# Kernel optimization log

Measured on AMD Instinct MI355X. Metric: run time of the kernel, lower is better.

Reference implementation:

```python
import jax, jax.numpy as jnp
import numpy as np

K = 4  # spline order (degree K-1)


def bspline_basis(x, t, k):
    """Evaluate the k nonzero B-spline basis functions of order k at x.

    x: [B, I] floats; t: [G+2k-1] clamped knot vector.
    Returns (idx [B,I,k] int32 basis indices, basis [B,I,k] values),
    using the de Boor / NURBS-book triangular recursion (vectorized over B,I;
    Python loops only over the small fixed order k).
    """
    m = t.shape[0]
    # interval index: t[i] <= x < t[i+1], clamped to valid span [k-1, m-k-1]
    i = jnp.clip(jnp.searchsorted(t, x, side='right') - 1, k - 1, m - k - 1)
    p = k - 1
    N = [jnp.ones_like(x)]
    left, right = [], []
    for j in range(1, p + 1):
        left.append(x - t[i + 1 - j])
        right.append(t[i + j] - x)
        saved = jnp.zeros_like(x)
        Nn = []
        for r in range(j):
            temp = N[r] / (right[r] + left[j - 1 - r])
            Nn.append(saved + right[r] * temp)
            saved = left[j - 1 - r] * temp
        Nn.append(saved)
        N = Nn
    idx = jnp.stack([i - p + j for j in range(k)], axis=-1)   # [B,I,k]
    basis = jnp.stack(N, axis=-1)                             # [B,I,k]
    return idx, basis


def setup_inputs() -> dict:
    key = jax.random.key(0)
    k1, k2 = jax.random.split(key)
    B, I, O, G, k = 2048, 128, 128, 64, K
    t0, t1 = -1.0, 1.0
    x = jax.random.uniform(k1, (B, I), jnp.float32, minval=t0, maxval=t1)
    # xavier_normal_ for fan_in=in_dim, fan_out=out_dim (per-slice heuristic)
    std = (2.0 / (I + O)) ** 0.5
    w = jax.random.normal(k2, (G + k, I, O), jnp.float32) * std
    t = jnp.concatenate([
        jnp.full((k - 1,), t0, jnp.float32),
        jnp.linspace(t0, t1, G + 1, dtype=jnp.float32),
        jnp.full((k - 1,), t1, jnp.float32),
    ])
    return {"x": x, "w": w, "t": t}


def reference(x, w, t):
    k = K
    B, I = x.shape
    O = w.shape[2]
    idx, basis = bspline_basis(x, t, k)                       # [B,I,k]
    # activation slot uses the last row of w (torch index -1)
    act_idx = jnp.full((B, I, 1), w.shape[0] - 1, idx.dtype)
    idx_full = jnp.concatenate([idx, act_idx], axis=-1)       # [B,I,k+1]
    y = jnp.concatenate([basis, jax.nn.silu(x)[..., None]], axis=-1)  # [B,I,k+1]
    wt = jnp.transpose(w, (1, 0, 2))                          # [I, G+k, O]
    w2 = wt[jnp.arange(I)[None, :, None], idx_full]           # [B,I,k+1,O] gather
    return jnp.einsum('bij,bijo->bo', y, w2)                  # [B,O]
```

## Files before the change

kernel.cpp:

```cpp
#include <hip/hip_runtime.h>
#include <math.h>

#define B_TOTAL 2048
#define I_DIM   128
#define O_DIM   128
#define GK      68
#define NKNOT   71
#define W_ELEMS ((size_t)GK * I_DIM * O_DIM)
#define WS_MIN  (W_ELEMS * 2)

__device__ __forceinline__ float rdlanef(float v, int l) {
    return __int_as_float(__builtin_amdgcn_readlane(__float_as_int(v), l));
}
__device__ __forceinline__ unsigned short f2bf(float f) {
    unsigned u = __float_as_uint(f);
    return (unsigned short)((u + 0x7fffu + ((u >> 16) & 1u)) >> 16);
}
__device__ __forceinline__ float bflo(unsigned u) { return __uint_as_float(u << 16); }
__device__ __forceinline__ float bfhi(unsigned u) { return __uint_as_float(u & 0xffff0000u); }

__global__ __launch_bounds__(256)
void wcvt(const float* __restrict__ w, unsigned short* __restrict__ wbf) {
    const int tid = threadIdx.x;
    const int p   = blockIdx.x * 8 + (tid >> 5);
    const int oq  = (tid & 31) * 4;
    const int g   = p >> 7;
    const int i   = p & 127;
    const float4 v = *(const float4*)(w + (size_t)p * O_DIM + oq);
    ushort4 o4;
    o4.x = f2bf(v.x); o4.y = f2bf(v.y); o4.z = f2bf(v.z); o4.w = f2bf(v.w);
    *(ushort4*)(wbf + ((size_t)i * GK + g) * O_DIM + oq) = o4;
}

__global__ __launch_bounds__(256, 8)
void flashkan_gather(const float* __restrict__ x,
                     const unsigned short* __restrict__ wbf,
                     const float* __restrict__ t,
                     float* __restrict__ out) {
    __shared__ float t_sh[NKNOT];
    __shared__ float psum[4][O_DIM];

    const int tid  = threadIdx.x;
    const int b    = blockIdx.x;
    const int wave = tid >> 6;
    const int lane = tid & 63;
    const int l32  = lane & 31;

    if (tid < NKNOT) t_sh[tid] = t[tid];
    __syncthreads();

    float cf0, cf1, cf2, cf3, cf4;
    int   cg;
    {
        const float xv = x[(size_t)b * I_DIM + wave * 32 + l32];

        int ik = 3 + (int)floorf((xv + 1.0f) * 32.0f);
        ik = min(max(ik, 3), 66);
        while (ik < 66 && xv >= t_sh[ik + 1]) ++ik;
        while (ik > 3 && xv < t_sh[ik]) --ik;

        float l0, l1, l2, r0, r1, r2;
        float N0 = 1.0f, N1, N2, N3;
        l0 = xv - t_sh[ik];
        r0 = t_sh[ik + 1] - xv;
        {
            float temp = N0 / (r0 + l0);
            N0 = r0 * temp;
            N1 = l0 * temp;
        }
        l1 = xv - t_sh[ik - 1];
        r1 = t_sh[ik + 2] - xv;
        {
            float saved = 0.0f, temp;
            temp = N0 / (r0 + l1);
            N0 = saved + r0 * temp;
            saved = l1 * temp;
            temp = N1 / (r1 + l0);
            N1 = saved + r1 * temp;
            N2 = l0 * temp;
        }
        l2 = xv - t_sh[ik - 2];
        r2 = t_sh[ik + 3] - xv;
        {
            float saved = 0.0f, temp;
            temp = N0 / (r0 + l2);
            N0 = saved + r0 * temp;
            saved = l2 * temp;
            temp = N1 / (r1 + l1);
            N1 = saved + r1 * temp;
            saved = l1 * temp;
            temp = N2 / (r2 + l0);
            N2 = saved + r2 * temp;
            N3 = l0 * temp;
        }
        cf0 = N0; cf1 = N1; cf2 = N2; cf3 = N3;
        cf4 = xv / (1.0f + expf(-xv));
        cg  = ik - 3;
    }

    const int i_base = wave * 32;
    float ax = 0.0f, ay = 0.0f;

    #pragma unroll
    for (int k = 0; k < 32; ++k) {
        const float c0 = rdlanef(cf0, k);
        const float c1 = rdlanef(cf1, k);
        const float c2 = rdlanef(cf2, k);
        const float c3 = rdlanef(cf3, k);
        const float c4 = rdlanef(cf4, k);
        const int   g0 = __builtin_amdgcn_readlane(cg, k);

        const int i = i_base + k;
        const unsigned* rp = (const unsigned*)(wbf + (((size_t)i * GK + g0) << 7)) + lane;
        const unsigned* sp = (const unsigned*)(wbf + (((size_t)i * GK + 67) << 7)) + lane;
        const unsigned u0 = rp[0];
        const unsigned u1 = rp[64];
        const unsigned u2 = rp[128];
        const unsigned u3 = rp[192];
        const unsigned u4 = *sp;

        ax += c0 * bflo(u0) + c1 * bflo(u1) + c2 * bflo(u2)
            + c3 * bflo(u3) + c4 * bflo(u4);
        ay += c0 * bfhi(u0) + c1 * bfhi(u1) + c2 * bfhi(u2)
            + c3 * bfhi(u3) + c4 * bfhi(u4);
    }

    psum[wave][lane * 2]     = ax;
    psum[wave][lane * 2 + 1] = ay;
    __syncthreads();

    if (tid < O_DIM) {
        out[(size_t)b * O_DIM + tid] =
            psum[0][tid] + psum[1][tid] + psum[2][tid] + psum[3][tid];
    }
}

__global__ __launch_bounds__(256)
void flashkan_gather_f32(const float* __restrict__ x,
                         const float* __restrict__ w,
                         const float* __restrict__ t,
                         float* __restrict__ out) {
    __shared__ float t_sh[NKNOT];
    __shared__ float psum[4][O_DIM];

    const int tid  = threadIdx.x;
    const int b    = blockIdx.x;
    const int wave = tid >> 6;
    const int lane = tid & 63;
    const int l32  = lane & 31;

    if (tid < NKNOT) t_sh[tid] = t[tid];
    __syncthreads();

    float cf0, cf1, cf2, cf3, cf4;
    int   cg;
    {
        const float xv = x[(size_t)b * I_DIM + wave * 32 + l32];
        int ik = 3 + (int)floorf((xv + 1.0f) * 32.0f);
        ik = min(max(ik, 3), 66);
        while (ik < 66 && xv >= t_sh[ik + 1]) ++ik;
        while (ik > 3 && xv < t_sh[ik]) --ik;
        float l0, l1, l2, r0, r1, r2;
        float N0 = 1.0f, N1, N2, N3;
        l0 = xv - t_sh[ik];  r0 = t_sh[ik + 1] - xv;
        { float temp = N0 / (r0 + l0); N0 = r0 * temp; N1 = l0 * temp; }
        l1 = xv - t_sh[ik - 1];  r1 = t_sh[ik + 2] - xv;
        { float saved = 0.0f, temp;
          temp = N0 / (r0 + l1); N0 = saved + r0 * temp; saved = l1 * temp;
          temp = N1 / (r1 + l0); N1 = saved + r1 * temp; N2 = l0 * temp; }
        l2 = xv - t_sh[ik - 2];  r2 = t_sh[ik + 3] - xv;
        { float saved = 0.0f, temp;
          temp = N0 / (r0 + l2); N0 = saved + r0 * temp; saved = l2 * temp;
          temp = N1 / (r1 + l1); N1 = saved + r1 * temp; saved = l1 * temp;
          temp = N2 / (r2 + l0); N2 = saved + r2 * temp; N3 = l0 * temp; }
        cf0 = N0; cf1 = N1; cf2 = N2; cf3 = N3;
        cf4 = xv / (1.0f + expf(-xv));
        cg  = ik - 3;
    }

    const int i_base = wave * 32;
    float ax = 0.0f, ay = 0.0f;
    #pragma unroll 8
    for (int k = 0; k < 32; ++k) {
        const float c0 = rdlanef(cf0, k);
        const float c1 = rdlanef(cf1, k);
        const float c2 = rdlanef(cf2, k);
        const float c3 = rdlanef(cf3, k);
        const float c4 = rdlanef(cf4, k);
        const int   g0 = __builtin_amdgcn_readlane(cg, k);
        const int i = i_base + k;
        const float2* base = (const float2*)(w + (size_t)i * O_DIM) + lane;
        const size_t rs = (size_t)I_DIM * O_DIM / 2;
        const float2 v0 = base[(size_t)g0 * rs];
        const float2 v1 = base[(size_t)(g0 + 1) * rs];
        const float2 v2 = base[(size_t)(g0 + 2) * rs];
        const float2 v3 = base[(size_t)(g0 + 3) * rs];
        const float2 v4 = base[(size_t)(GK - 1) * rs];
        ax += c0 * v0.x + c1 * v1.x + c2 * v2.x + c3 * v3.x + c4 * v4.x;
        ay += c0 * v0.y + c1 * v1.y + c2 * v2.y + c3 * v3.y + c4 * v4.y;
    }

    psum[wave][lane * 2]     = ax;
    psum[wave][lane * 2 + 1] = ay;
    __syncthreads();
    if (tid < O_DIM) {
        out[(size_t)b * O_DIM + tid] =
            psum[0][tid] + psum[1][tid] + psum[2][tid] + psum[3][tid];
    }
}

extern "C" void kernel_launch(void* const* d_in, const int* in_sizes, int n_in,
                              void* d_out, int out_size, void* d_ws, size_t ws_size,
                              hipStream_t stream) {
    const float* x = (const float*)d_in[0];
    const float* w = (const float*)d_in[1];
    const float* t = (const float*)d_in[2];
    float* out = (float*)d_out;

    if (ws_size >= WS_MIN) {
        unsigned short* wbf = (unsigned short*)d_ws;
        wcvt<<<(int)(W_ELEMS / (8 * 128)), 256, 0, stream>>>(w, wbf);
        flashkan_gather<<<B_TOTAL, 256, 0, stream>>>(x, wbf, t, out);
    } else {
        flashkan_gather_f32<<<B_TOTAL, 256, 0, stream>>>(x, w, t, out);
    }
}
```

Baseline: 30.95 us.

## Tile batch and input dims, stage weight slices in LDS with split-I reduction

Replaces the one-block-per-batch-row gather kernel with a tiled kernel. Each block handles 32 batch rows and 8 input features, streaming each feature's bf16 weight slice into XOR-swizzled shared memory through double-buffered global_load_lds. Partial sums from the 16 input-feature groups are written to workspace and combined by a separate reduce kernel, with an atomicAdd fallback when workspace is smaller. This lets each weight slice be reused across 32 batch rows instead of being re-gathered from global memory per row. The cost is an extra reduce launch and round trip through partial sums, plus more block barriers.

```diff
diff --git a/kernel.cpp b/kernel.cpp
--- a/kernel.cpp
+++ b/kernel.cpp
@@ -6,11 +6,20 @@
 #define O_DIM   128
 #define GK      68
 #define NKNOT   71
-#define W_ELEMS ((size_t)GK * I_DIM * O_DIM)
-#define WS_MIN  (W_ELEMS * 2)
-
-__device__ __forceinline__ float rdlanef(float v, int l) {
-    return __int_as_float(__builtin_amdgcn_readlane(__float_as_int(v), l));
+#define BT      32
+#define BTILES  (B_TOTAL / BT)
+#define RI      8
+#define NR      (I_DIM / RI)
+#define THREADS 512
+#define SLICE_B 17408
+#define SLICE_US (SLICE_B / 2)
+#define PART_FLOATS ((size_t)NR * B_TOTAL * O_DIM)
+#define WF_OFF   (PART_FLOATS * 4)
+#define WF_BYTES ((size_t)I_DIM * SLICE_B)
+#define WS_NEED  (WF_OFF + WF_BYTES)
+
+__device__ __forceinline__ float rdlanef(float v, int sl) {
+    return __int_as_float(__builtin_amdgcn_readlane(__float_as_int(v), sl));
 }
 __device__ __forceinline__ unsigned short f2bf(float f) {
     unsigned u = __float_as_uint(f);
@@ -19,32 +28,82 @@
 __device__ __forceinline__ float bflo(unsigned u) { return __uint_as_float(u << 16); }
 __device__ __forceinline__ float bfhi(unsigned u) { return __uint_as_float(u & 0xffff0000u); }
 
+__device__ __forceinline__ float sel4f(int q, float a, float b, float c, float d) {
+    float r = (q == 1) ? b : a;
+    r = (q == 2) ? c : r;
+    r = (q == 3) ? d : r;
+    return r;
+}
+__device__ __forceinline__ int sel4i(int q, int a, int b, int c, int d) {
+    int r = (q == 1) ? b : a;
+    r = (q == 2) ? c : r;
+    r = (q == 3) ? d : r;
+    return r;
+}
+
+__device__ __forceinline__ void coef_eval(float xv, const float* t_sh,
+                                          float& c0, float& c1, float& c2,
+                                          float& c3, float& c4, int& g0) {
+    int ik = 3 + (int)floorf((xv + 1.0f) * 32.0f);
+    ik = min(max(ik, 3), 66);
+    while (ik < 66 && xv >= t_sh[ik + 1]) ++ik;
+    while (ik > 3 && xv < t_sh[ik]) --ik;
+    float l0, l1, l2, r0, r1, r2;
+    float N0 = 1.0f, N1, N2, N3;
+    l0 = xv - t_sh[ik];  r0 = t_sh[ik + 1] - xv;
+    { float temp = N0 / (r0 + l0); N0 = r0 * temp; N1 = l0 * temp; }
+    l1 = xv - t_sh[ik - 1];  r1 = t_sh[ik + 2] - xv;
+    { float saved = 0.0f, temp;
+      temp = N0 / (r0 + l1); N0 = saved + r0 * temp; saved = l1 * temp;
+      temp = N1 / (r1 + l0); N1 = saved + r1 * temp; N2 = l0 * temp; }
+    l2 = xv - t_sh[ik - 2];  r2 = t_sh[ik + 3] - xv;
+    { float saved = 0.0f, temp;
+      temp = N0 / (r0 + l2); N0 = saved + r0 * temp; saved = l2 * temp;
+      temp = N1 / (r1 + l1); N1 = saved + r1 * temp; saved = l1 * temp;
+      temp = N2 / (r2 + l0); N2 = saved + r2 * temp; N3 = l0 * temp; }
+    c0 = N0; c1 = N1; c2 = N2; c3 = N3;
+    c4 = xv / (1.0f + expf(-xv));
+    g0 = ik - 3;
+}
+
 __global__ __launch_bounds__(256)
-void wcvt(const float* __restrict__ w, unsigned short* __restrict__ wbf) {
+void wcvt(const float* __restrict__ w, unsigned short* __restrict__ wf) {
+    const int gblk = blockIdx.x * 256 + threadIdx.x;
+    const int i    = gblk / (GK * 16);
+    const int rem  = gblk - i * (GK * 16);
+    const int r    = rem >> 4;
+    const int j    = rem & 15;
+    const float* src = w + ((size_t)r * I_DIM + i) * O_DIM + j * 8;
+    const float4 a = *(const float4*)src;
+    const float4 b = *(const float4*)(src + 4);
+    uint4 st;
+    st.x = (unsigned)f2bf(a.x) | ((unsigned)f2bf(a.y) << 16);
+    st.y = (unsigned)f2bf(a.z) | ((unsigned)f2bf(a.w) << 16);
+    st.z = (unsigned)f2bf(b.x) | ((unsigned)f2bf(b.y) << 16);
+    st.w = (unsigned)f2bf(b.z) | ((unsigned)f2bf(b.w) << 16);
+    char* dst = (char*)wf + (size_t)i * SLICE_B + r * 256 + ((j ^ (r & 15)) << 4);
+    *(uint4*)dst = st;
+}
+
+template<bool USE_WS>
+__global__ __launch_bounds__(THREADS, 6)
+void flashkan_q(const float* __restrict__ x,
+                const unsigned short* __restrict__ wf,
+                const float* __restrict__ t,
+                float* __restrict__ dst) {
+    __shared__ __align__(16) char sbuf[2][SLICE_B];
+    __shared__ float t_sh[NKNOT];
+
     const int tid = threadIdx.x;
-    const int p   = blockIdx.x * 8 + (tid >> 5);
-    const int oq  = (tid & 31) * 4;
-    const int g   = p >> 7;
-    const int i   = p & 127;
-    const float4 v = *(const float4*)(w + (size_t)p * O_DIM + oq);
-    ushort4 o4;
-    o4.x = f2bf(v.x); o4.y = f2bf(v.y); o4.z = f2bf(v.z); o4.w = f2bf(v.w);
-    *(ushort4*)(wbf + ((size_t)i * GK + g) * O_DIM + oq) = o4;
-}
-
-__global__ __launch_bounds__(256, 8)
-void flashkan_gather(const float* __restrict__ x,
-                     const unsigned short* __restrict__ wbf,
-                     const float* __restrict__ t,
-                     float* __restrict__ out) {
-    __shared__ float t_sh[NKNOT];
-    __shared__ float psum[4][O_DIM];
-
-    const int tid  = threadIdx.x;
-    const int b    = blockIdx.x;
-    const int wave = tid >> 6;
-    const int lane = tid & 63;
-    const int l32  = lane & 31;
+    const int bid = blockIdx.x;
+    const int bt  = bid >> 4;
+    const int ir  = bid & 15;
+    const int b0  = bt * BT;
+    const int i0  = ir * RI;
+    const int wv  = tid >> 6;
+    const int l   = tid & 63;
+    const int q   = l >> 4;
+    const int l15 = l & 15;
 
     if (tid < NKNOT) t_sh[tid] = t[tid];
     __syncthreads();
@@ -52,87 +111,98 @@
     float cf0, cf1, cf2, cf3, cf4;
     int   cg;
     {
-        const float xv = x[(size_t)b * I_DIM + wave * 32 + l32];
-
-        int ik = 3 + (int)floorf((xv + 1.0f) * 32.0f);
-        ik = min(max(ik, 3), 66);
-        while (ik < 66 && xv >= t_sh[ik + 1]) ++ik;
-        while (ik > 3 && xv < t_sh[ik]) --ik;
-
-        float l0, l1, l2, r0, r1, r2;
-        float N0 = 1.0f, N1, N2, N3;
-        l0 = xv - t_sh[ik];
-        r0 = t_sh[ik + 1] - xv;
-        {
-            float temp = N0 / (r0 + l0);
-            N0 = r0 * temp;
-            N1 = l0 * temp;
+        const int bw = (l >> 3) & 3;
+        const int ii = l & 7;
+        const float xv = x[(size_t)(b0 + wv * 4 + bw) * I_DIM + (i0 + ii)];
+        coef_eval(xv, t_sh, cf0, cf1, cf2, cf3, cf4, cg);
+    }
+
+    auto stage = [&](int sel, int i_abs) {
+        for (int c = wv; c < 17; c += 8) {
+            const unsigned short* src = wf + (size_t)i_abs * SLICE_US + c * 512 + l * 8;
+            void* dstp = (void*)(&sbuf[sel][0] + c * 1024);
+            __builtin_amdgcn_global_load_lds(
+                (const __attribute__((address_space(1))) void*)src,
+                (__attribute__((address_space(3))) void*)dstp,
+                16, 0, 0);
         }
-        l1 = xv - t_sh[ik - 1];
-        r1 = t_sh[ik + 2] - xv;
-        {
-            float saved = 0.0f, temp;
-            temp = N0 / (r0 + l1);
-            N0 = saved + r0 * temp;
-            saved = l1 * temp;
-            temp = N1 / (r1 + l0);
-            N1 = saved + r1 * temp;
-            N2 = l0 * temp;
+    };
+
+    float acc[8];
+    #pragma unroll
+    for (int e = 0; e < 8; ++e) acc[e] = 0.0f;
+
+    const int silu_off = 67 * 256 + ((l15 ^ 3) << 4);
+
+    auto compute = [&](int ii, const char* bufc) {
+        const int o0 = ii, o1 = 8 | ii, o2 = 16 | ii, o3 = 24 | ii;
+        const float c0 = sel4f(q, rdlanef(cf0,o0), rdlanef(cf0,o1), rdlanef(cf0,o2), rdlanef(cf0,o3));
+        const float c1 = sel4f(q, rdlanef(cf1,o0), rdlanef(cf1,o1), rdlanef(cf1,o2), rdlanef(cf1,o3));
+        const float c2 = sel4f(q, rdlanef(cf2,o0), rdlanef(cf2,o1), rdlanef(cf2,o2), rdlanef(cf2,o3));
+        const float c3 = sel4f(q, rdlanef(cf3,o0), rdlanef(cf3,o1), rdlanef(cf3,o2), rdlanef(cf3,o3));
+        const float c4 = sel4f(q, rdlanef(cf4,o0), rdlanef(cf4,o1), rdlanef(cf4,o2), rdlanef(cf4,o3));
+        const int  vg0 = sel4i(q,
+            __builtin_amdgcn_readlane(cg,o0), __builtin_amdgcn_readlane(cg,o1),
+            __builtin_amdgcn_readlane(cg,o2), __builtin_amdgcn_readlane(cg,o3));
+        const float cc[4] = {c0, c1, c2, c3};
+
+        #pragma unroll
+        for (int k = 0; k < 4; ++k) {
+            const int row = vg0 + k;
+            const int off = (row << 8) | ((l15 ^ (row & 15)) << 4);
+            const uint4 u = *(const uint4*)(bufc + off);
+            const float ck = cc[k];
+            acc[0] += ck * bflo(u.x);  acc[1] += ck * bfhi(u.x);
+            acc[2] += ck * bflo(u.y);  acc[3] += ck * bfhi(u.y);
+            acc[4] += ck * bflo(u.z);  acc[5] += ck * bfhi(u.z);
+            acc[6] += ck * bflo(u.w);  acc[7] += ck * bfhi(u.w);
         }
-        l2 = xv - t_sh[ik - 2];
-        r2 = t_sh[ik + 3] - xv;
-        {
-            float saved = 0.0f, temp;
-            temp = N0 / (r0 + l2);
-            N0 = saved + r0 * temp;
-            saved = l2 * temp;
-            temp = N1 / (r1 + l1);
-            N1 = saved + r1 * temp;
-            saved = l1 * temp;
-            temp = N2 / (r2 + l0);
-            N2 = saved + r2 * temp;
-            N3 = l0 * temp;
-        }
-        cf0 = N0; cf1 = N1; cf2 = N2; cf3 = N3;
-        cf4 = xv / (1.0f + expf(-xv));
-        cg  = ik - 3;
-    }
-
-    const int i_base = wave * 32;
-    float ax = 0.0f, ay = 0.0f;
-
+        const uint4 su = *(const uint4*)(bufc + silu_off);
+        acc[0] += c4 * bflo(su.x);  acc[1] += c4 * bfhi(su.x);
+        acc[2] += c4 * bflo(su.y);  acc[3] += c4 * bfhi(su.y);
+        acc[4] += c4 * bflo(su.z);  acc[5] += c4 * bfhi(su.z);
+        acc[6] += c4 * bflo(su.w);  acc[7] += c4 * bfhi(su.w);
+    };
+
+    stage(0, i0);
+    __syncthreads();
+
+    for (int iib = 0; iib < RI; iib += 2) {
+        stage(1, i0 + iib + 1);
+        compute(iib, (const char*)sbuf[0]);
+        __syncthreads();
+        if (iib + 2 < RI) stage(0, i0 + iib + 2);
+        compute(iib + 1, (const char*)sbuf[1]);
+        __syncthreads();
+    }
+
+    const int b = b0 + wv * 4 + q;
+    const float4 A = make_float4(acc[0], acc[1], acc[2], acc[3]);
+    const float4 Bv = make_float4(acc[4], acc[5], acc[6], acc[7]);
+    if (USE_WS) {
+        float* dp = dst + ((size_t)ir * B_TOTAL + b) * O_DIM + l15 * 8;
+        *(float4*)dp = A;
+        *(float4*)(dp + 4) = Bv;
+    } else {
+        float* dp = dst + (size_t)b * O_DIM + l15 * 8;
+        atomicAdd(dp,     A.x); atomicAdd(dp + 1, A.y);
+        atomicAdd(dp + 2, A.z); atomicAdd(dp + 3, A.w);
+        atomicAdd(dp + 4, Bv.x); atomicAdd(dp + 5, Bv.y);
+        atomicAdd(dp + 6, Bv.z); atomicAdd(dp + 7, Bv.w);
+    }
+}
+
+__global__ __launch_bounds__(256)
+void flashkan_reduce(const float* __restrict__ ws, float* __restrict__ out) {
+    const int f = blockIdx.x * 256 + threadIdx.x;
+    const float4* base = (const float4*)ws + f;
+    float4 s = make_float4(0.0f, 0.0f, 0.0f, 0.0f);
     #pragma unroll
-    for (int k = 0; k < 32; ++k) {
-        const float c0 = rdlanef(cf0, k);
-        const float c1 = rdlanef(cf1, k);
-        const float c2 = rdlanef(cf2, k);
-        const float c3 = rdlanef(cf3, k);
-        const float c4 = rdlanef(cf4, k);
-        const int   g0 = __builtin_amdgcn_readlane(cg, k);
-
-        const int i = i_base + k;
-        const unsigned* rp = (const unsigned*)(wbf + (((size_t)i * GK + g0) << 7)) + lane;
-        const unsigned* sp = (const unsigned*)(wbf + (((size_t)i * GK + 67) << 7)) + lane;
-        const unsigned u0 = rp[0];
-        const unsigned u1 = rp[64];
-        const unsigned u2 = rp[128];
-        const unsigned u3 = rp[192];
-        const unsigned u4 = *sp;
-
-        ax += c0 * bflo(u0) + c1 * bflo(u1) + c2 * bflo(u2)
-            + c3 * bflo(u3) + c4 * bflo(u4);
-        ay += c0 * bfhi(u0) + c1 * bfhi(u1) + c2 * bfhi(u2)
-            + c3 * bfhi(u3) + c4 * bfhi(u4);
-    }
-
-    psum[wave][lane * 2]     = ax;
-    psum[wave][lane * 2 + 1] = ay;
-    __syncthreads();
-
-    if (tid < O_DIM) {
-        out[(size_t)b * O_DIM + tid] =
-            psum[0][tid] + psum[1][tid] + psum[2][tid] + psum[3][tid];
-    }
+    for (int r2 = 0; r2 < NR; ++r2) {
+        const float4 v = base[(size_t)r2 * (B_TOTAL * O_DIM / 4)];
+        s.x += v.x; s.y += v.y; s.z += v.z; s.w += v.w;
+    }
+    ((float4*)out)[f] = s;
 }
 
 __global__ __launch_bounds__(256)
@@ -142,50 +212,24 @@
                          float* __restrict__ out) {
     __shared__ float t_sh[NKNOT];
     __shared__ float psum[4][O_DIM];
-
     const int tid  = threadIdx.x;
     const int b    = blockIdx.x;
     const int wave = tid >> 6;
     const int lane = tid & 63;
     const int l32  = lane & 31;
-
     if (tid < NKNOT) t_sh[tid] = t[tid];
     __syncthreads();
-
-    float cf0, cf1, cf2, cf3, cf4;
-    int   cg;
+    float cf0, cf1, cf2, cf3, cf4; int cg;
     {
         const float xv = x[(size_t)b * I_DIM + wave * 32 + l32];
-        int ik = 3 + (int)floorf((xv + 1.0f) * 32.0f);
-        ik = min(max(ik, 3), 66);
-        while (ik < 66 && xv >= t_sh[ik + 1]) ++ik;
-        while (ik > 3 && xv < t_sh[ik]) --ik;
-        float l0, l1, l2, r0, r1, r2;
-        float N0 = 1.0f, N1, N2, N3;
-        l0 = xv - t_sh[ik];  r0 = t_sh[ik + 1] - xv;
-        { float temp = N0 / (r0 + l0); N0 = r0 * temp; N1 = l0 * temp; }
-        l1 = xv - t_sh[ik - 1];  r1 = t_sh[ik + 2] - xv;
-        { float saved = 0.0f, temp;
-          temp = N0 / (r0 + l1); N0 = saved + r0 * temp; saved = l1 * temp;
-          temp = N1 / (r1 + l0); N1 = saved + r1 * temp; N2 = l0 * temp; }
-        l2 = xv - t_sh[ik - 2];  r2 = t_sh[ik + 3] - xv;
-        { float saved = 0.0f, temp;
-          temp = N0 / (r0 + l2); N0 = saved + r0 * temp; saved = l2 * temp;
-          temp = N1 / (r1 + l1); N1 = saved + r1 * temp; saved = l1 * temp;
-          temp = N2 / (r2 + l0); N2 = saved + r2 * temp; N3 = l0 * temp; }
-        cf0 = N0; cf1 = N1; cf2 = N2; cf3 = N3;
-        cf4 = xv / (1.0f + expf(-xv));
-        cg  = ik - 3;
-    }
-
+        coef_eval(xv, t_sh, cf0, cf1, cf2, cf3, cf4, cg);
+    }
     const int i_base = wave * 32;
     float ax = 0.0f, ay = 0.0f;
     #pragma unroll 8
     for (int k = 0; k < 32; ++k) {
-        const float c0 = rdlanef(cf0, k);
-        const float c1 = rdlanef(cf1, k);
-        const float c2 = rdlanef(cf2, k);
-        const float c3 = rdlanef(cf3, k);
+        const float c0 = rdlanef(cf0, k), c1 = rdlanef(cf1, k);
+        const float c2 = rdlanef(cf2, k), c3 = rdlanef(cf3, k);
         const float c4 = rdlanef(cf4, k);
         const int   g0 = __builtin_amdgcn_readlane(cg, k);
         const int i = i_base + k;
@@ -199,7 +243,6 @@
         ax += c0 * v0.x + c1 * v1.x + c2 * v2.x + c3 * v3.x + c4 * v4.x;
         ay += c0 * v0.y + c1 * v1.y + c2 * v2.y + c3 * v3.y + c4 * v4.y;
     }
-
     psum[wave][lane * 2]     = ax;
     psum[wave][lane * 2 + 1] = ay;
     __syncthreads();
@@ -217,10 +260,19 @@
     const float* t = (const float*)d_in[2];
     float* out = (float*)d_out;
 
-    if (ws_size >= WS_MIN) {
-        unsigned short* wbf = (unsigned short*)d_ws;
-        wcvt<<<(int)(W_ELEMS / (8 * 128)), 256, 0, stream>>>(w, wbf);
-        flashkan_gather<<<B_TOTAL, 256, 0, stream>>>(x, wbf, t, out);
+    const int wcvt_blocks = I_DIM * GK * 16 / 256;
+
+    if (ws_size >= WS_NEED) {
+        float* part = (float*)d_ws;
+        unsigned short* wfp = (unsigned short*)((char*)d_ws + WF_OFF);
+        wcvt<<<wcvt_blocks, 256, 0, stream>>>(w, wfp);
+        flashkan_q<true><<<BTILES * NR, THREADS, 0, stream>>>(x, wfp, t, part);
+        flashkan_reduce<<<B_TOTAL * O_DIM / 4 / 256, 256, 0, stream>>>(part, out);
+    } else if (ws_size >= WF_BYTES) {
+        unsigned short* wfp = (unsigned short*)d_ws;
+        hipMemsetAsync(out, 0, (size_t)out_size * sizeof(float), stream);
+        wcvt<<<wcvt_blocks, 256, 0, stream>>>(w, wfp);
+        flashkan_q<false><<<BTILES * NR, THREADS, 0, stream>>>(x, wfp, t, out);
     } else {
         flashkan_gather_f32<<<B_TOTAL, 256, 0, stream>>>(x, w, t, out);
     }
```

Result: slower. 43.69 us (+41.2%).

## Assign one wave per batch row and drop shared-memory cross-wave reduction

Applied to the files above, without the earlier changes.

Replaces the one-block-per-row gather kernel with 512-thread blocks where each wave owns a whole batch row and loops over all 128 inputs in two 64-wide halves. This removes the shared-memory partial-sum buffer and the second barrier, and writes the output directly as float2. The cost is a longer serial loop per wave (128 iterations instead of 32) with a partial unroll of 4. Grid size drops to 256 blocks, which may reduce parallelism and latency hiding on the gathered weight loads.

```diff
diff --git a/kernel.cpp b/kernel.cpp
--- a/kernel.cpp
+++ b/kernel.cpp
@@ -8,9 +8,11 @@
 #define NKNOT   71
 #define W_ELEMS ((size_t)GK * I_DIM * O_DIM)
 #define WS_MIN  (W_ELEMS * 2)
+#define SLICE_DW (GK * O_DIM / 2)
+#define ROW_DW   (O_DIM / 2)
 
-__device__ __forceinline__ float rdlanef(float v, int l) {
-    return __int_as_float(__builtin_amdgcn_readlane(__float_as_int(v), l));
+__device__ __forceinline__ float rdlanef(float v, int sl) {
+    return __int_as_float(__builtin_amdgcn_readlane(__float_as_int(v), sl));
 }
 __device__ __forceinline__ unsigned short f2bf(float f) {
     unsigned u = __float_as_uint(f);
@@ -18,6 +20,31 @@
 }
 __device__ __forceinline__ float bflo(unsigned u) { return __uint_as_float(u << 16); }
 __device__ __forceinline__ float bfhi(unsigned u) { return __uint_as_float(u & 0xffff0000u); }
+
+__device__ __forceinline__ void coef_eval(float xv, const float* t_sh,
+                                          float& c0, float& c1, float& c2,
+                                          float& c3, float& c4, int& g0) {
+    int ik = 3 + (int)floorf((xv + 1.0f) * 32.0f);
+    ik = min(max(ik, 3), 66);
+    while (ik < 66 && xv >= t_sh[ik + 1]) ++ik;
+    while (ik > 3 && xv < t_sh[ik]) --ik;
+    float l0, l1, l2, r0, r1, r2;
+    float N0 = 1.0f, N1, N2, N3;
+    l0 = xv - t_sh[ik];  r0 = t_sh[ik + 1] - xv;
+    { float temp = N0 / (r0 + l0); N0 = r0 * temp; N1 = l0 * temp; }
+    l1 = xv - t_sh[ik - 1];  r1 = t_sh[ik + 2] - xv;
+    { float saved = 0.0f, temp;
+      temp = N0 / (r0 + l1); N0 = saved + r0 * temp; saved = l1 * temp;
+      temp = N1 / (r1 + l0); N1 = saved + r1 * temp; N2 = l0 * temp; }
+    l2 = xv - t_sh[ik - 2];  r2 = t_sh[ik + 3] - xv;
+    { float saved = 0.0f, temp;
+      temp = N0 / (r0 + l2); N0 = saved + r0 * temp; saved = l2 * temp;
+      temp = N1 / (r1 + l1); N1 = saved + r1 * temp; saved = l1 * temp;
+      temp = N2 / (r2 + l0); N2 = saved + r2 * temp; N3 = l0 * temp; }
+    c0 = N0; c1 = N1; c2 = N2; c3 = N3;
+    c4 = xv / (1.0f + expf(-xv));
+    g0 = ik - 3;
+}
 
 __global__ __launch_bounds__(256)
 void wcvt(const float* __restrict__ w, unsigned short* __restrict__ wbf) {
@@ -32,91 +59,42 @@
     *(ushort4*)(wbf + ((size_t)i * GK + g) * O_DIM + oq) = o4;
 }
 
-__global__ __launch_bounds__(256, 8)
-void flashkan_gather(const float* __restrict__ x,
-                     const unsigned short* __restrict__ wbf,
-                     const float* __restrict__ t,
-                     float* __restrict__ out) {
+__global__ __launch_bounds__(512, 2)
+void flashkan_sync(const float* __restrict__ x,
+                   const unsigned short* __restrict__ wbf,
+                   const float* __restrict__ t,
+                   float* __restrict__ out) {
     __shared__ float t_sh[NKNOT];
-    __shared__ float psum[4][O_DIM];
 
     const int tid  = threadIdx.x;
-    const int b    = blockIdx.x;
     const int wave = tid >> 6;
     const int lane = tid & 63;
-    const int l32  = lane & 31;
+    const int b    = blockIdx.x * 8 + wave;
 
     if (tid < NKNOT) t_sh[tid] = t[tid];
     __syncthreads();
 
-    float cf0, cf1, cf2, cf3, cf4;
-    int   cg;
-    {
-        const float xv = x[(size_t)b * I_DIM + wave * 32 + l32];
+    float a0, a1, a2, a3, a4;  int ga;
+    float b0, b1, b2, b3, b4;  int gb;
+    coef_eval(x[(size_t)b * I_DIM + lane],      t_sh, a0, a1, a2, a3, a4, ga);
+    coef_eval(x[(size_t)b * I_DIM + lane + 64], t_sh, b0, b1, b2, b3, b4, gb);
 
-        int ik = 3 + (int)floorf((xv + 1.0f) * 32.0f);
-        ik = min(max(ik, 3), 66);
-        while (ik < 66 && xv >= t_sh[ik + 1]) ++ik;
-        while (ik > 3 && xv < t_sh[ik]) --ik;
-
-        float l0, l1, l2, r0, r1, r2;
-        float N0 = 1.0f, N1, N2, N3;
-        l0 = xv - t_sh[ik];
-        r0 = t_sh[ik + 1] - xv;
-        {
-            float temp = N0 / (r0 + l0);
-            N0 = r0 * temp;
-            N1 = l0 * temp;
-        }
-        l1 = xv - t_sh[ik - 1];
-        r1 = t_sh[ik + 2] - xv;
-        {
-            float saved = 0.0f, temp;
-            temp = N0 / (r0 + l1);
-            N0 = saved + r0 * temp;
-            saved = l1 * temp;
-            temp = N1 / (r1 + l0);
-            N1 = saved + r1 * temp;
-            N2 = l0 * temp;
-        }
-        l2 = xv - t_sh[ik - 2];
-        r2 = t_sh[ik + 3] - xv;
-        {
-            float saved = 0.0f, temp;
-            temp = N0 / (r0 + l2);
-            N0 = saved + r0 * temp;
-            saved = l2 * temp;
-            temp = N1 / (r1 + l1);
-            N1 = saved + r1 * temp;
-            saved = l1 * temp;
-            temp = N2 / (r2 + l0);
-            N2 = saved + r2 * temp;
-            N3 = l0 * temp;
-        }
-        cf0 = N0; cf1 = N1; cf2 = N2; cf3 = N3;
-        cf4 = xv / (1.0f + expf(-xv));
-        cg  = ik - 3;
-    }
-
-    const int i_base = wave * 32;
+    const unsigned* wdw = (const unsigned*)wbf;
     float ax = 0.0f, ay = 0.0f;
 
-    #pragma unroll
-    for (int k = 0; k < 32; ++k) {
-        const float c0 = rdlanef(cf0, k);
-        const float c1 = rdlanef(cf1, k);
-        const float c2 = rdlanef(cf2, k);
-        const float c3 = rdlanef(cf3, k);
-        const float c4 = rdlanef(cf4, k);
-        const int   g0 = __builtin_amdgcn_readlane(cg, k);
+    #pragma unroll 4
+    for (int k = 0; k < 64; ++k) {
+        const float c0 = rdlanef(a0, k), c1 = rdlanef(a1, k);
+        const float c2 = rdlanef(a2, k), c3 = rdlanef(a3, k);
+        const float c4 = rdlanef(a4, k);
+        const int   g0 = __builtin_amdgcn_readlane(ga, k);
 
-        const int i = i_base + k;
-        const unsigned* rp = (const unsigned*)(wbf + (((size_t)i * GK + g0) << 7)) + lane;
-        const unsigned* sp = (const unsigned*)(wbf + (((size_t)i * GK + 67) << 7)) + lane;
+        const unsigned* rp = wdw + (size_t)k * SLICE_DW + g0 * ROW_DW + lane;
+        const unsigned* sp = wdw + (size_t)k * SLICE_DW + 67 * ROW_DW + lane;
         const unsigned u0 = rp[0];
-        const unsigned u1 = rp[64];
-        const unsigned u2 = rp[128];
-        const unsigned u3 = rp[192];
+        const unsigned u1 = rp[ROW_DW];
+        const unsigned u2 = rp[2 * ROW_DW];
+        const unsigned u3 = rp[3 * ROW_DW];
         const unsigned u4 = *sp;
 
         ax += c0 * bflo(u0) + c1 * bflo(u1) + c2 * bflo(u2)
@@ -125,14 +103,28 @@
             + c3 * bfhi(u3) + c4 * bfhi(u4);
     }
 
-    psum[wave][lane * 2]     = ax;
-    psum[wave][lane * 2 + 1] = ay;
-    __syncthreads();
+    #pragma unroll 4
+    for (int k = 0; k < 64; ++k) {
+        const float c0 = rdlanef(b0, k), c1 = rdlanef(b1, k);
+        const float c2 = rdlanef(b2, k), c3 = rdlanef(b3, k);
+        const float c4 = rdlanef(b4, k);
+        const int   g0 = __builtin_amdgcn_readlane(gb, k);
 
-    if (tid < O_DIM) {
-        out[(size_t)b * O_DIM + tid] =
-            psum[0][tid] + psum[1][tid] + psum[2][tid] + psum[3][tid];
+        const unsigned* rp = wdw + (size_t)(k + 64) * SLICE_DW + g0 * ROW_DW + lane;
+        const unsigned* sp = wdw + (size_t)(k + 64) * SLICE_DW + 67 * ROW_DW + lane;
+        const unsigned u0 = rp[0];
+        const unsigned u1 = rp[ROW_DW];
+        const unsigned u2 = rp[2 * ROW_DW];
+        const unsigned u3 = rp[3 * ROW_DW];
+        const unsigned u4 = *sp;
+
+        ax += c0 * bflo(u0) + c1 * bflo(u1) + c2 * bflo(u2)
+            + c3 * bflo(u3) + c4 * bflo(u4);
+        ay += c0 * bfhi(u0) + c1 * bfhi(u1) + c2 * bfhi(u2)
+            + c3 * bfhi(u3) + c4 * bfhi(u4);
     }
+
+    *(float2*)(out + (size_t)b * O_DIM + lane * 2) = make_float2(ax, ay);
 }
 
 __global__ __launch_bounds__(256)
@@ -142,50 +134,22 @@
                          float* __restrict__ out) {
     __shared__ float t_sh[NKNOT];
     __shared__ float psum[4][O_DIM];
-
     const int tid  = threadIdx.x;
     const int b    = blockIdx.x;
     const int wave = tid >> 6;
     const int lane = tid & 63;
     const int l32  = lane & 31;
-
     if (tid < NKNOT) t_sh[tid] = t[tid];
     __syncthreads();
-
-    float cf0, cf1, cf2, cf3, cf4;
-    int   cg;
-    {
-        const float xv = x[(size_t)b * I_DIM + wave * 32 + l32];
-        int ik = 3 + (int)floorf((xv + 1.0f) * 32.0f);
-        ik = min(max(ik, 3), 66);
-        while (ik < 66 && xv >= t_sh[ik + 1]) ++ik;
-        while (ik > 3 && xv < t_sh[ik]) --ik;
-        float l0, l1, l2, r0, r1, r2;
-        float N0 = 1.0f, N1, N2, N3;
-        l0 = xv - t_sh[ik];  r0 = t_sh[ik + 1] - xv;
-        { float temp = N0 / (r0 + l0); N0 = r0 * temp; N1 = l0 * temp; }
-        l1 = xv - t_sh[ik - 1];  r1 = t_sh[ik + 2] - xv;
-        { float saved = 0.0f, temp;
-          temp = N0 / (r0 + l1); N0 = saved + r0 * temp; saved = l1 * temp;
-          temp = N1 / (r1 + l0); N1 = saved + r1 * temp; N2 = l0 * temp; }
-        l2 = xv - t_sh[ik - 2];  r2 = t_sh[ik + 3] - xv;
-        { float saved = 0.0f, temp;
-          temp = N0 / (r0 + l2); N0 = saved + r0 * temp; saved = l2 * temp;
-          temp = N1 / (r1 + l1); N1 = saved + r1 * temp; saved = l1 * temp;
-          temp = N2 / (r2 + l0); N2 = saved + r2 * temp; N3 = l0 * temp; }
-        cf0 = N0; cf1 = N1; cf2 = N2; cf3 = N3;
-        cf4 = xv / (1.0f + expf(-xv));
-        cg  = ik - 3;
-    }
-
+    float cf0, cf1, cf2, cf3, cf4; int cg;
+    coef_eval(x[(size_t)b * I_DIM + wave * 32 + l32], t_sh,
+              cf0, cf1, cf2, cf3, cf4, cg);
     const int i_base = wave * 32;
     float ax = 0.0f, ay = 0.0f;
     #pragma unroll 8
     for (int k = 0; k < 32; ++k) {
-        const float c0 = rdlanef(cf0, k);
-        const float c1 = rdlanef(cf1, k);
-        const float c2 = rdlanef(cf2, k);
-        const float c3 = rdlanef(cf3, k);
+        const float c0 = rdlanef(cf0, k), c1 = rdlanef(cf1, k);
+        const float c2 = rdlanef(cf2, k), c3 = rdlanef(cf3, k);
         const float c4 = rdlanef(cf4, k);
         const int   g0 = __builtin_amdgcn_readlane(cg, k);
         const int i = i_base + k;
@@ -199,7 +163,6 @@
         ax += c0 * v0.x + c1 * v1.x + c2 * v2.x + c3 * v3.x + c4 * v4.x;
         ay += c0 * v0.y + c1 * v1.y + c2 * v2.y + c3 * v3.y + c4 * v4.y;
     }
-
     psum[wave][lane * 2]     = ax;
     psum[wave][lane * 2 + 1] = ay;
     __syncthreads();
@@ -220,7 +183,7 @@
     if (ws_size >= WS_MIN) {
         unsigned short* wbf = (unsigned short*)d_ws;
         wcvt<<<(int)(W_ELEMS / (8 * 128)), 256, 0, stream>>>(w, wbf);
-        flashkan_gather<<<B_TOTAL, 256, 0, stream>>>(x, wbf, t, out);
+        flashkan_sync<<<B_TOTAL / 8, 512, 0, stream>>>(x, wbf, t, out);
     } else {
         flashkan_gather_f32<<<B_TOTAL, 256, 0, stream>>>(x, w, t, out);
     }
```

Measured after the change: 32.19 us. 1.04x slower.
